# Performance work log

Hardware: AMD Instinct MI355X
Metric: run time of the kernel (lower is better)

Reference implementation:

```python
import jax, jax.numpy as jnp
import numpy as np

B, C_IN, FH, TW = 64, 8, 128, 128
FBINS, A, M_ARR, M_SRC = 257, 360, 4, 2
EPS = 1e-6


def _conv2d(x, w):
    return jax.lax.conv_general_dilated(x, w, (1, 1), 'SAME', dimension_numbers=('NCHW', 'OIHW', 'NCHW'))


def _bn(x, g, b, m, v):
    sh = (1, -1, 1, 1)
    return (x - m.reshape(sh)) * jax.lax.rsqrt(v.reshape(sh) + 1e-5) * g.reshape(sh) + b.reshape(sh)


def _pool2(x):
    b_, c, h, w = x.shape
    return x.reshape(b_, c, h // 2, 2, w // 2, 2).max(axis=(3, 5))


def _block(x, w, g, b, m, v):
    return _pool2(jax.nn.relu(_bn(_conv2d(x, w), g, b, m, v)))


def _conv1d(x, w, b):
    return jax.lax.conv_general_dilated(x, w, (1,), 'SAME', dimension_numbers=('NCH', 'OIH', 'NCH')) + b[None, :, None]


def setup_inputs() -> dict:
    ks = jax.random.split(jax.random.key(0), 16)
    r = lambda i, shp, s=1.0: jax.random.normal(ks[i], shp, dtype=jnp.float32) * s
    d = {
        'X': r(0, (B, C_IN, FH, TW)),
        'sv_real': r(1, (B, FBINS, A, M_ARR)),
        'sv_imag': r(2, (B, FBINS, A, M_ARR)),
        'correlation': jnp.zeros((1,), jnp.float32),
        'conv1_w': r(3, (64, C_IN, 3, 3), 0.1),
        'conv2_w': r(4, (64, 64, 3, 3), 0.04),
        'conv3_w': r(5, (64, 64, 3, 3), 0.04),
        'conv4_w': r(6, (FBINS, 64, 3, 3), 0.04),
        'fc_w': r(7, (32, 64), 0.1),
        'fc_b': jnp.zeros((32,), jnp.float32),
        'convs2_w': r(8, (FBINS, FBINS, 3), 0.02),
        'convs2_b': jnp.zeros((FBINS,), jnp.float32),
        'convs1_w': r(9, (1, FBINS, 3), 0.03),
        'convs1_b': jnp.zeros((1,), jnp.float32),
        'ca_w1': r(10, (16, FBINS), 0.06),
        'ca_w2': r(11, (FBINS, 16), 0.2),
    }
    for i, c in [(1, 64), (2, 64), (3, 64), (4, FBINS)]:
        d[f'bn{i}_g'] = jnp.ones((c,), jnp.float32)
        d[f'bn{i}_b'] = jnp.zeros((c,), jnp.float32)
        d[f'bn{i}_m'] = jnp.zeros((c,), jnp.float32)
        d[f'bn{i}_v'] = jnp.ones((c,), jnp.float32)
    return d


def reference(X, sv_real, sv_imag, correlation,
              conv1_w, bn1_g, bn1_b, bn1_m, bn1_v,
              conv2_w, bn2_g, bn2_b, bn2_m, bn2_v,
              conv3_w, bn3_g, bn3_b, bn3_m, bn3_v,
              conv4_w, bn4_g, bn4_b, bn4_m, bn4_v,
              fc_w, fc_b, convs2_w, convs2_b, convs1_w, convs1_b,
              ca_w1, ca_w2):
    b_ = X.shape[0]
    # CNN encoder: (B,8,128,128) -> (B,257,8,8)
    z = _block(X, conv1_w, bn1_g, bn1_b, bn1_m, bn1_v)
    z = _block(z, conv2_w, bn2_g, bn2_b, bn2_m, bn2_v)
    z = _block(z, conv3_w, bn3_g, bn3_b, bn3_m, bn3_v)
    z = _block(z, conv4_w, bn4_g, bn4_b, bn4_m, bn4_v)
    z = z.reshape(b_, FBINS, -1) @ fc_w.T + fc_b            # (B,257,32)
    z = z.reshape(b_, FBINS, C_IN // 2, C_IN)               # (B,257,4,8)
    Rz = jax.lax.complex(z[..., :M_ARR], z[..., M_ARR:])    # (B,257,4,4)
    # hermitianize + diagonal loading
    Rz = 0.5 * (Rz + jnp.conj(jnp.swapaxes(Rz, -1, -2)))
    Rz = Rz + 1e-5 * jnp.eye(M_ARR, dtype=Rz.dtype)
    _, evecs = jnp.linalg.eigh(Rz)                          # ascending eigenvalues
    Un = evecs[..., ::-1][..., M_SRC:]                      # noise subspace (B,F,4,2)
    UnUnH = Un @ jnp.conj(jnp.swapaxes(Un, -1, -2))         # (B,F,4,4)
    svc = jnp.conj(jax.lax.complex(sv_real, sv_imag))       # (B,F,A,4)
    # faithful to torch code: denom[a] = sum_{m,n} conj(sv[a,m]) UnUnH[m,n] conj(sv[a,n])
    denom = jnp.real(jnp.einsum('bfam,bfmn,bfan->bfa', svc, UnUnH, svc))
    spectrum = 1.0 / jnp.maximum(denom, EPS)                # (B,257,360)
    spectrum = jax.nn.leaky_relu(_conv1d(spectrum, convs2_w, convs2_b), 0.1)
    # channel attention over the 257 freq channels
    y = spectrum.mean(-1)                                   # (B,257)
    att = jax.nn.sigmoid(jax.nn.relu(y @ ca_w1.T) @ ca_w2.T)
    spectrum = spectrum * att[:, :, None]
    spectrum = jax.nn.sigmoid(_conv1d(spectrum, convs1_w, convs1_b))[:, 0, :]  # (B,360)
    # soft-argmax over top-5 peaks
    angles = jnp.linspace(0.0, 360.0, A + 1)[:-1]
    vals, idx = jax.lax.top_k(spectrum, 5)
    wts = jax.nn.softmax(20.0 * vals, axis=-1)
    doa = (wts * angles[idx]).sum(-1)[:, None]              # (B,1)
    return doa, spectrum
```

## Files before the change

### kernel.cpp

```cpp
#include <hip/hip_runtime.h>

typedef unsigned short u16;
typedef unsigned int u32;
typedef short short8 __attribute__((ext_vector_type(8)));
typedef float f32x4 __attribute__((ext_vector_type(4)));

#define NB 64
#define NFB 257
#define NANG 360

__device__ __forceinline__ u16 f2bf(float x) {
    u32 u = __float_as_uint(x);
    u = (u + 0x7fffu + ((u >> 16) & 1u)) >> 16;
    return (u16)u;
}
__device__ __forceinline__ float bf2f(u16 h) { return __uint_as_float(((u32)h) << 16); }

__global__ __launch_bounds__(256) void bnprep(
    const float* g1, const float* b1, const float* m1, const float* v1,
    const float* g2, const float* b2, const float* m2, const float* v2,
    const float* g3, const float* b3, const float* m3, const float* v3,
    const float* g4, const float* b4, const float* m4, const float* v4,
    float* out)
{
    int L = blockIdx.x;
    const float* gs[4] = {g1, g2, g3, g4};
    const float* bs[4] = {b1, b2, b3, b4};
    const float* ms[4] = {m1, m2, m3, m4};
    const float* vs[4] = {v1, v2, v3, v4};
    int n = (L == 3) ? 257 : 64;
    float* sc = out + L * 1024;
    float* bi = sc + 512;
    for (int i = threadIdx.x; i < n; i += 256) {
        float s = gs[L][i] * rsqrtf(vs[L][i] + 1e-5f);
        sc[i] = s;
        bi[i] = bs[L][i] - ms[L][i] * s;
    }
}

__global__ __launch_bounds__(256) void bpack(
    const float* __restrict__ w, u16* __restrict__ Bp,
    int CREAL, int OCREAL, int NT, int KCC, int NFTOT)
{
    int i = blockIdx.x * 256 + threadIdx.x;
    int total = NT * KCC * 2 * NFTOT * 64;
    if (i >= total) return;
    int lane = i & 63;
    int t = i >> 6;
    int nf = t % NFTOT;
    int th = t / NFTOT;
    int h = th & 1;
    int chunk = th >> 1;
    int s = chunk / KCC, kc = chunk % KCC;
    int n = nf * 16 + (lane & 15);
    int k0 = kc * 32 + (lane >> 4) * 8;
    u16 o8[8];
    #pragma unroll
    for (int e = 0; e < 8; ++e) {
        int k = k0 + e;
        float v = 0.f;
        if (k < CREAL && n < OCREAL) v = w[((size_t)n * CREAL + k) * NT + s];
        u16 hh = f2bf(v);
        o8[e] = (h == 0) ? hh : f2bf(v - bf2f(hh));
    }
    u16* d = Bp + (size_t)i * 8;
    #pragma unroll
    for (int e = 0; e < 8; ++e) d[e] = o8[e];
}

__global__ __launch_bounds__(256) void bpack1(const float* __restrict__ w, u16* __restrict__ Bp)
{
    int i = blockIdx.x * 256 + threadIdx.x;
    if (i >= 3 * 2 * 4 * 64) return;
    int lane = i & 63;
    int t = i >> 6;
    int nf = t % 4;
    int th = t / 4;
    int h = th & 1;
    int ky = th >> 1;
    int n = nf * 16 + (lane & 15);
    int q = lane >> 4;
    u16 o8[8];
    #pragma unroll
    for (int e = 0; e < 8; ++e) {
        float v = (q < 3) ? w[((size_t)(n * 8 + e) * 3 + ky) * 3 + q] : 0.f;
        u16 hh = f2bf(v);
        o8[e] = (h == 0) ? hh : f2bf(v - bf2f(hh));
    }
    u16* d = Bp + (size_t)i * 8;
    #pragma unroll
    for (int e = 0; e < 8; ++e) d[e] = o8[e];
}

__global__ __launch_bounds__(256) void xpack_kernel(
    const float* __restrict__ X, u16* __restrict__ hi, u16* __restrict__ lo)
{
    __shared__ float Xs[8][132];
    int bid = blockIdx.x;
    int prow = bid % 130;
    int b = bid / 130;
    bool inr = (prow >= 1 && prow <= 128);
    for (int i = threadIdx.x; i < 8 * 130; i += 256) {
        int c = i / 130, pcol = i % 130;
        float v = 0.f;
        if (inr && pcol >= 1 && pcol <= 128)
            v = X[(((size_t)b * 8 + c) * 128 + (prow - 1)) * 128 + (pcol - 1)];
        Xs[c][pcol] = v;
    }
    __syncthreads();
    for (int p = threadIdx.x; p < 130; p += 256) {
        short8 h8, l8;
        #pragma unroll
        for (int c = 0; c < 8; ++c) {
            float f = Xs[c][p];
            u16 hh = f2bf(f);
            h8[c] = (short)hh;
            l8[c] = (short)f2bf(f - bf2f(hh));
        }
        size_t o = (((size_t)b * 130 + prow) * 130 + p) * 8;
        *(short8*)(hi + o) = h8;
        *(short8*)(lo + o) = l8;
    }
}

__global__ __launch_bounds__(256) void zpad(
    u16* hi, u16* lo, int Bn, int Hp, int Wp, int Cb, int doCols)
{
    int perB = 2 * Wp + (doCols ? 2 * (Hp - 2) : 0);
    long total = (long)Bn * perB * Cb;
    for (long idx = blockIdx.x * 256L + threadIdx.x; idx < total; idx += (long)gridDim.x * 256) {
        int c = (int)(idx % Cb);
        long t = idx / Cb;
        int p = (int)(t % perB);
        int b = (int)(t / perB);
        int row, col;
        if (p < Wp) { row = 0; col = p; }
        else if (p < 2 * Wp) { row = Hp - 1; col = p - Wp; }
        else { int pp = p - 2 * Wp; row = 1 + (pp >> 1); col = (pp & 1) ? (Wp - 1) : 0; }
        size_t o = (((size_t)b * Hp + row) * Wp + col) * Cb + c;
        hi[o] = 0;
        lo[o] = 0;
    }
}

__global__ __launch_bounds__(256) void conv_c1(
    const u16* __restrict__ Ahi, const u16* __restrict__ Alo,
    const u16* __restrict__ Bp,
    const float* __restrict__ esc, const float* __restrict__ ebi,
    u16* __restrict__ Ohi, u16* __restrict__ Olo)
{
    constexpr int Wst = 130, Hp = 130;
    constexpr int SROWS = 5;
    constexpr int SPIX = SROWS * Wst;
    constexpr int PSTR = 48;
    constexpr int STAGEB = SPIX * PSTR;
    constexpr int POOLB = 2 * 128 * 64 * 4;
    __shared__ __align__(16) char sm[POOLB + 64];

    int bid = blockIdx.x;
    int ytile = bid % 64;
    int b = bid / 64;
    int y0 = ytile * 2;
    int tid = threadIdx.x;
    int wv = tid >> 6;
    int l = tid & 63;
    int r = l & 15, q = l >> 4;

    for (int pix = tid; pix < SPIX; pix += 256) {
        int prow = y0 + pix / Wst, pcol = pix % Wst;
        uint4 vh = {0, 0, 0, 0}, vl = {0, 0, 0, 0};
        if (prow < Hp) {
            size_t g = (((size_t)b * Hp + prow) * Wst + pcol) * 16;
            vh = *(const uint4*)((const char*)Ahi + g);
            vl = *(const uint4*)((const char*)Alo + g);
        }
        *(uint4*)(sm + pix * PSTR) = vh;
        *(uint4*)(sm + STAGEB + pix * PSTR) = vl;
    }
    __syncthreads();

    f32x4 acc[4][4];
    #pragma unroll
    for (int mi = 0; mi < 4; ++mi)
        #pragma unroll
        for (int ni = 0; ni < 4; ++ni)
            acc[mi][ni] = (f32x4){0.f, 0.f, 0.f, 0.f};

    #pragma unroll
    for (int ky = 0; ky < 3; ++ky) {
        short8 ah[4], al[4];
        #pragma unroll
        for (int mi = 0; mi < 4; ++mi) {
            int mp0 = (wv * 4 + mi) * 16;
            int mpix = ((mp0 >> 7) + ky) * Wst + (mp0 & 127);
            int off = (mpix + r + q) * PSTR;
            ah[mi] = *(const short8*)(sm + off);
            al[mi] = *(const short8*)(sm + STAGEB + off);
        }
        #pragma unroll
        for (int ni = 0; ni < 4; ++ni) {
            const u16* bt = Bp + ((size_t)(ky * 2) * 4 + ni) * 512 + l * 8;
            short8 bh = *(const short8*)bt;
            short8 bl = *(const short8*)(bt + 4 * 512);
            #pragma unroll
            for (int mi = 0; mi < 4; ++mi) {
                acc[mi][ni] = __builtin_amdgcn_mfma_f32_16x16x32_bf16(ah[mi], bh, acc[mi][ni], 0, 0, 0);
                acc[mi][ni] = __builtin_amdgcn_mfma_f32_16x16x32_bf16(ah[mi], bl, acc[mi][ni], 0, 0, 0);
                acc[mi][ni] = __builtin_amdgcn_mfma_f32_16x16x32_bf16(al[mi], bh, acc[mi][ni], 0, 0, 0);
            }
        }
    }

    __syncthreads();
    float* pt = (float*)sm;
    #pragma unroll
    for (int mi = 0; mi < 4; ++mi)
        #pragma unroll
        for (int ni = 0; ni < 4; ++ni)
            #pragma unroll
            for (int j = 0; j < 4; ++j) {
                int mp = (wv * 4 + mi) * 16 + q * 4 + j;
                pt[mp * 64 + ni * 16 + r] = acc[mi][ni][j];
            }
    __syncthreads();
    for (int i = tid; i < 64 * 64; i += 256) {
        int c = i % 64;
        int x2 = i / 64;
        float sc0 = esc[c], bi0 = ebi[c];
        float m = -3.4e38f;
        #pragma unroll
        for (int dy = 0; dy < 2; ++dy)
            #pragma unroll
            for (int dx = 0; dx < 2; ++dx) {
                float v = fmaf(pt[(dy * 128 + 2 * x2 + dx) * 64 + c], sc0, bi0);
                m = fmaxf(m, v);
            }
        m = fmaxf(m, 0.f);
        size_t o = (((size_t)b * 66 + (y0 / 2 + 1)) * 66 + (x2 + 1)) * 64 + c;
        u16 hh = f2bf(m);
        Ohi[o] = hh;
        Olo[o] = f2bf(m - bf2f(hh));
    }
}

template<int C, int H, int W, int OC, int R, int KH, int KW, int NF, int MFW,
         int PSTR, int OUTMODE, int NFTOT, int CSECT>
__global__ __launch_bounds__(256) void conv_gemm(
    const u16* __restrict__ Ahi, const u16* __restrict__ Alo,
    const u16* __restrict__ Bp,
    const float* __restrict__ esc, const float* __restrict__ ebi,
    u16* __restrict__ Ohi, u16* __restrict__ Olo, float* __restrict__ Of)
{
    constexpr int KCC = (C + 31) / 32;
    constexpr int KCS = KCC / CSECT;
    constexpr int SECB = (C / CSECT) * 2;
    constexpr int CB16 = SECB / 16;
    constexpr int Wst = W + KW - 1;
    constexpr int Hp = H + KH - 1;
    constexpr int SROWS = R + KH - 1;
    constexpr int SPIX = SROWS * Wst;
    constexpr int OCB = NF * 16;
    constexpr int HT = (H + R - 1) / R;
    constexpr int STAGEB = SPIX * PSTR;
    constexpr int POOLB = (OUTMODE == 2) ? 0 : (R * W * OCB * 4);
    constexpr int SMEMB = (2 * STAGEB > POOLB) ? (2 * STAGEB) : POOLB;
    __shared__ __align__(16) char sm[SMEMB + 64];

    int bid = blockIdx.x;
    int ytile = bid % HT;
    int b = bid / HT;
    int tid = threadIdx.x;
    int wv = tid >> 6;
    int l = tid & 63;
    int r = l & 15, q = l >> 4;
    int y0 = ytile * R;

    f32x4 acc[MFW][NF];
    #pragma unroll
    for (int mi = 0; mi < MFW; ++mi)
        #pragma unroll
        for (int ni = 0; ni < NF; ++ni)
            acc[mi][ni] = (f32x4){0.f, 0.f, 0.f, 0.f};

    for (int cs = 0; cs < CSECT; ++cs) {
        __syncthreads();
        for (int i = tid; i < SPIX * CB16; i += 256) {
            int pix = i / CB16, sub = i - pix * CB16;
            int prow = y0 + pix / Wst, pcol = pix % Wst;
            uint4 vh = {0, 0, 0, 0}, vl = {0, 0, 0, 0};
            if (prow < Hp) {
                size_t g = (((size_t)b * Hp + prow) * Wst + pcol) * (size_t)(C * 2)
                         + (size_t)cs * SECB + (size_t)sub * 16;
                vh = *(const uint4*)((const char*)Ahi + g);
                vl = *(const uint4*)((const char*)Alo + g);
            }
            *(uint4*)(sm + pix * PSTR + sub * 16) = vh;
            *(uint4*)(sm + STAGEB + pix * PSTR + sub * 16) = vl;
        }
        __syncthreads();

        for (int s = 0; s < KH * KW; ++s) {
            int ky = s / KW, kx = s % KW;
            #pragma unroll
            for (int kc = 0; kc < KCS; ++kc) {
                int chunk = s * KCC + cs * KCS + kc;
                short8 ah[MFW], al[MFW];
                #pragma unroll
                for (int mi = 0; mi < MFW; ++mi) {
                    int mp0 = (wv * MFW + mi) * 16;
                    int mpix = ((mp0 / W) + ky) * Wst + (mp0 % W) + kx;
                    int off = (mpix + r) * PSTR + q * 16 + kc * 64;
                    ah[mi] = *(const short8*)(sm + off);
                    al[mi] = *(const short8*)(sm + STAGEB + off);
                }
                #pragma unroll
                for (int ni = 0; ni < NF; ++ni) {
                    int nfg = blockIdx.y * NF + ni;
                    const u16* bt = Bp + ((size_t)(chunk * 2) * NFTOT + nfg) * 512 + l * 8;
                    short8 bh = *(const short8*)bt;
                    short8 bl = *(const short8*)(bt + (size_t)NFTOT * 512);
                    #pragma unroll
                    for (int mi = 0; mi < MFW; ++mi) {
                        acc[mi][ni] = __builtin_amdgcn_mfma_f32_16x16x32_bf16(ah[mi], bh, acc[mi][ni], 0, 0, 0);
                        acc[mi][ni] = __builtin_amdgcn_mfma_f32_16x16x32_bf16(ah[mi], bl, acc[mi][ni], 0, 0, 0);
                        acc[mi][ni] = __builtin_amdgcn_mfma_f32_16x16x32_bf16(al[mi], bh, acc[mi][ni], 0, 0, 0);
                    }
                }
            }
        }
    }

    if (OUTMODE == 2) {
        #pragma unroll
        for (int ni = 0; ni < NF; ++ni) {
            int nn = (blockIdx.y * NF + ni) * 16 + r;
            float bi0 = (nn < OC) ? ebi[nn] : 0.f;
            #pragma unroll
            for (int mi = 0; mi < MFW; ++mi) {
                #pragma unroll
                for (int j = 0; j < 4; ++j) {
                    int t = y0 + (wv * MFW + mi) * 16 + q * 4 + j;
                    if (t < H && nn < OC) {
                        float v = acc[mi][ni][j] + bi0;
                        Of[((size_t)b * H + t) * (size_t)OC + nn] = (v >= 0.f) ? v : 0.1f * v;
                    }
                }
            }
        }
    } else {
        __syncthreads();
        float* pt = (float*)sm;
        #pragma unroll
        for (int mi = 0; mi < MFW; ++mi)
            #pragma unroll
            for (int ni = 0; ni < NF; ++ni)
                #pragma unroll
                for (int j = 0; j < 4; ++j) {
                    int mp = (wv * MFW + mi) * 16 + q * 4 + j;
                    pt[mp * OCB + ni * 16 + r] = acc[mi][ni][j];
                }
        __syncthreads();
        constexpr int HO = H / 2, WO = W / 2;
        for (int i = tid; i < (R / 2) * WO * OCB; i += 256) {
            int c = i % OCB;
            int rem = i / OCB;
            int x2 = rem % WO;
            int y2 = rem / WO;
            int oc = blockIdx.y * OCB + c;
            float sc0 = 0.f, bi0 = 0.f;
            if (oc < OC) { sc0 = esc[oc]; bi0 = ebi[oc]; }
            float m = -3.4e38f;
            #pragma unroll
            for (int dy = 0; dy < 2; ++dy)
                #pragma unroll
                for (int dx = 0; dx < 2; ++dx) {
                    float v = fmaf(pt[((2 * y2 + dy) * W + 2 * x2 + dx) * OCB + c], sc0, bi0);
                    m = fmaxf(m, v);
                }
            m = fmaxf(m, 0.f);
            if (OUTMODE == 0) {
                size_t o = (((size_t)b * (HO + 2) + (y0 / 2 + y2 + 1)) * (WO + 2) + (x2 + 1)) * (size_t)OC + oc;
                u16 hh = f2bf(m);
                Ohi[o] = hh;
                Olo[o] = f2bf(m - bf2f(hh));
            } else {
                if (oc < OC)
                    Of[(((size_t)b * HO + (y0 / 2 + y2)) * WO + x2) * (size_t)OC + oc] = m;
            }
        }
    }
}

__global__ __launch_bounds__(512) void convs2_gemm(
    const u16* __restrict__ Ahi, const u16* __restrict__ Alo,
    const u16* __restrict__ Bp, const float* __restrict__ bia,
    float* __restrict__ sp2)
{
    constexpr int SPIX = 386;
    constexpr int PSTR = 80;
    constexpr int STAGEB = SPIX * PSTR;
    __shared__ __align__(16) char sm[2 * STAGEB];

    int b = blockIdx.x;
    int nt = blockIdx.y;
    int tid = threadIdx.x;
    int wv = tid >> 6;
    int l = tid & 63;
    int r = l & 15, q = l >> 4;

    f32x4 acc[3][3];
    #pragma unroll
    for (int mi = 0; mi < 3; ++mi)
        #pragma unroll
        for (int ni = 0; ni < 3; ++ni)
            acc[mi][ni] = (f32x4){0.f, 0.f, 0.f, 0.f};

    for (int cs = 0; cs < 9; ++cs) {
        __syncthreads();
        for (int i = tid; i < SPIX * 4; i += 512) {
            int pix = i >> 2, sub = i & 3;
            uint4 vh = {0, 0, 0, 0}, vl = {0, 0, 0, 0};
            if (pix < 362) {
                size_t g = ((size_t)b * 362 + pix) * 576 + (size_t)cs * 64 + (size_t)sub * 16;
                vh = *(const uint4*)((const char*)Ahi + g);
                vl = *(const uint4*)((const char*)Alo + g);
            }
            *(uint4*)(sm + pix * PSTR + sub * 16) = vh;
            *(uint4*)(sm + STAGEB + pix * PSTR + sub * 16) = vl;
        }
        __syncthreads();

        #pragma unroll
        for (int ky = 0; ky < 3; ++ky) {
            int chunk = ky * 9 + cs;
            short8 bh[3], bl[3];
            #pragma unroll
            for (int ni = 0; ni < 3; ++ni) {
                const u16* bt = Bp + ((size_t)(chunk * 2) * 18 + nt * 3 + ni) * 512 + l * 8;
                bh[ni] = *(const short8*)bt;
                bl[ni] = *(const short8*)(bt + 18 * 512);
            }
            #pragma unroll
            for (int mi = 0; mi < 3; ++mi) {
                int off = ((wv * 3 + mi) * 16 + r + ky) * PSTR + q * 16;
                short8 ah = *(const short8*)(sm + off);
                short8 al = *(const short8*)(sm + STAGEB + off);
                #pragma unroll
                for (int ni = 0; ni < 3; ++ni) {
                    acc[mi][ni] = __builtin_amdgcn_mfma_f32_16x16x32_bf16(ah, bh[ni], acc[mi][ni], 0, 0, 0);
                    acc[mi][ni] = __builtin_amdgcn_mfma_f32_16x16x32_bf16(ah, bl[ni], acc[mi][ni], 0, 0, 0);
                    acc[mi][ni] = __builtin_amdgcn_mfma_f32_16x16x32_bf16(al, bh[ni], acc[mi][ni], 0, 0, 0);
                }
            }
        }
    }

    #pragma unroll
    for (int ni = 0; ni < 3; ++ni) {
        int n = (nt * 3 + ni) * 16 + r;
        if (n >= NFB) continue;
        float bi0 = bia[n];
        #pragma unroll
        for (int mi = 0; mi < 3; ++mi) {
            int t0 = (wv * 3 + mi) * 16 + q * 4;
            #pragma unroll
            for (int j = 0; j < 4; ++j) {
                int t = t0 + j;
                if (t < NANG) {
                    float v = acc[mi][ni][j] + bi0;
                    sp2[((size_t)b * NANG + t) * NFB + n] = (v >= 0.f) ? v : 0.1f * v;
                }
            }
        }
    }
}

__global__ __launch_bounds__(256) void fc_kernel(
    const float* __restrict__ z, const float* __restrict__ fw,
    const float* __restrict__ fb, float* __restrict__ zfc)
{
    int bid = blockIdx.x;
    int ftile = bid % 33;
    int b = bid / 33;
    int j = threadIdx.x & 31;
    int f = ftile * 8 + (threadIdx.x >> 5);
    if (f >= 257) return;
    const float* zb = z + (size_t)b * 16448;
    float a = fb[j];
    #pragma unroll 8
    for (int s = 0; s < 64; ++s) a = fmaf(zb[s * 257 + f], fw[j * 64 + s], a);
    zfc[((size_t)b * 257 + f) * 32 + j] = a;
}

__global__ __launch_bounds__(64) void eigh_kernel(const float* __restrict__ z, double* __restrict__ rp)
{
    int idx = blockIdx.x * 64 + threadIdx.x;
    if (idx >= NB * NFB) return;
    const float* zr = z + (size_t)idx * 32;
    double Ar[4][4], Ai[4][4], Vr[4][4], Vi[4][4];
    #pragma unroll
    for (int m = 0; m < 4; ++m)
        #pragma unroll
        for (int n = 0; n < 4; ++n) {
            Ar[m][n] = 0.5 * ((double)zr[m * 8 + n] + (double)zr[n * 8 + m]);
            Ai[m][n] = 0.5 * ((double)zr[m * 8 + n + 4] - (double)zr[n * 8 + m + 4]);
            Vr[m][n] = (m == n) ? 1.0 : 0.0;
            Vi[m][n] = 0.0;
        }
    #pragma unroll
    for (int m = 0; m < 4; ++m) Ar[m][m] += 1e-5;

    for (int sweep = 0; sweep < 8; ++sweep) {
        #pragma unroll
        for (int p = 0; p < 3; ++p)
            #pragma unroll
            for (int qq = p + 1; qq < 4; ++qq) {
                double apr = Ar[p][qq], api = Ai[p][qq];
                double rmod = sqrt(apr * apr + api * api);
                if (rmod < 1e-300) continue;
                double cph = apr / rmod, sph = api / rmod;
                double tau = (Ar[qq][qq] - Ar[p][p]) / (2.0 * rmod);
                double t = (tau >= 0.0) ? (-1.0 / (tau + sqrt(1.0 + tau * tau)))
                                        : (1.0 / (-tau + sqrt(1.0 + tau * tau)));
                double c = 1.0 / sqrt(1.0 + t * t);
                double s = t * c;
                double wr = s * cph, wi = s * sph;
                #pragma unroll
                for (int i = 0; i < 4; ++i) {
                    double xr = Ar[i][p], xi = Ai[i][p];
                    double yr = Ar[i][qq], yi = Ai[i][qq];
                    Ar[i][p] = c * xr + (wr * yr + wi * yi);
                    Ai[i][p] = c * xi + (wr * yi - wi * yr);
                    Ar[i][qq] = c * yr - (wr * xr - wi * xi);
                    Ai[i][qq] = c * yi - (wr * xi + wi * xr);
                }
                #pragma unroll
                for (int i = 0; i < 4; ++i) {
                    double xr = Ar[p][i], xi = Ai[p][i];
                    double yr = Ar[qq][i], yi = Ai[qq][i];
                    Ar[p][i] = c * xr + (wr * yr - wi * yi);
                    Ai[p][i] = c * xi + (wr * yi + wi * yr);
                    Ar[qq][i] = c * yr - (wr * xr + wi * xi);
                    Ai[qq][i] = c * yi - (wr * xi - wi * xr);
                }
                #pragma unroll
                for (int i = 0; i < 4; ++i) {
                    double xr = Vr[i][p], xi = Vi[i][p];
                    double yr = Vr[i][qq], yi = Vi[i][qq];
                    Vr[i][p] = c * xr + (wr * yr + wi * yi);
                    Vi[i][p] = c * xi + (wr * yi - wi * yr);
                    Vr[i][qq] = c * yr - (wr * xr - wi * xi);
                    Vi[i][qq] = c * yi - (wr * xi + wi * xr);
                }
            }
    }
    double ev[4] = {Ar[0][0], Ar[1][1], Ar[2][2], Ar[3][3]};
    int i0 = 0;
    #pragma unroll
    for (int k = 1; k < 4; ++k) if (ev[k] < ev[i0]) i0 = k;
    int i1 = (i0 == 0) ? 1 : 0;
    #pragma unroll
    for (int k = 0; k < 4; ++k) if (k != i0 && ev[k] < ev[i1]) i1 = k;
    double* o = rp + (size_t)idx * 16;
    #pragma unroll
    for (int m = 0; m < 4; ++m)
        #pragma unroll
        for (int n = 0; n < 4; ++n)
            o[m * 4 + n] = Vr[m][i0] * Vr[n][i0] + Vi[m][i0] * Vi[n][i0]
                         + Vr[m][i1] * Vr[n][i1] + Vi[m][i1] * Vi[n][i1];
}

__global__ __launch_bounds__(256) void music_kernel(
    const float4* __restrict__ svr, const float4* __restrict__ svi,
    const double* __restrict__ rp, u16* __restrict__ muhi, u16* __restrict__ mulo)
{
    __shared__ double P[32][16];
    __shared__ float T[32][33];
    int bid = blockIdx.x;
    int at = bid % 12; bid /= 12;
    int ft = bid % 9;
    int b = bid / 9;
    int f0 = ft * 32, a0 = at * 32;
    int tid = threadIdx.x;
    for (int i = tid; i < 32 * 16; i += 256) {
        int fi = i >> 4, j = i & 15;
        int f = f0 + fi;
        P[fi][j] = (f < 257) ? rp[((size_t)b * 257 + f) * 16 + j] : 0.0;
    }
    __syncthreads();
    int asub = tid & 31, fsub = tid >> 5;
    int a = a0 + asub;
    #pragma unroll
    for (int k2 = 0; k2 < 4; ++k2) {
        int fl = fsub + 8 * k2;
        int f = f0 + fl;
        float val = 0.f;
        if (a < 360 && f < 257) {
            float4 u = svr[((size_t)b * 257 + f) * 360 + a];
            float4 w = svi[((size_t)b * 257 + f) * 360 + a];
            const double* Pf = P[fl];
            double ua[4] = {u.x, u.y, u.z, u.w};
            double wa[4] = {w.x, w.y, w.z, w.w};
            double qa = 0.0, qb = 0.0;
            #pragma unroll
            for (int m = 0; m < 4; ++m)
                #pragma unroll
                for (int n = 0; n < 4; ++n) {
                    double pmn = Pf[m * 4 + n];
                    qa += pmn * ua[m] * ua[n];
                    qb += pmn * wa[m] * wa[n];
                }
            double den = qa - qb;
            val = (float)(1.0 / fmax(den, 1e-6));
        }
        T[asub][fl] = val;
    }
    __syncthreads();
    #pragma unroll
    for (int p = 0; p < 4; ++p) {
        int row = p * 8 + (tid >> 5);
        int fc = tid & 31;
        int a2 = a0 + row;
        if (a2 < 360) {
            float v = T[row][fc];
            size_t o = (((size_t)b * 362) + a2 + 1) * 288 + f0 + fc;
            u16 hh = f2bf(v);
            muhi[o] = hh;
            mulo[o] = f2bf(v - bf2f(hh));
        }
    }
}

__global__ __launch_bounds__(256) void attn_partial(const float* __restrict__ sp2, float* __restrict__ part)
{
    int bid = blockIdx.x;
    int ch = bid % 6;
    int b = bid / 6;
    int t0 = ch * 60;
    for (int f = threadIdx.x; f < 257; f += 256) {
        float s = 0.f;
        for (int t = 0; t < 60; ++t) s += sp2[((size_t)b * 360 + t0 + t) * 257 + f];
        part[((size_t)b * 6 + ch) * 257 + f] = s;
    }
}

__global__ __launch_bounds__(256) void attn_finish(
    const float* __restrict__ part, const float* __restrict__ w1,
    const float* __restrict__ w2, float* __restrict__ att)
{
    __shared__ float ys[257];
    __shared__ float hs[16];
    int b = blockIdx.x;
    int tid = threadIdx.x;
    for (int f = tid; f < 257; f += 256) {
        float s = 0.f;
        #pragma unroll
        for (int c = 0; c < 6; ++c) s += part[((size_t)b * 6 + c) * 257 + f];
        ys[f] = s * (1.0f / 360.0f);
    }
    __syncthreads();
    if (tid < 16) {
        float h = 0.f;
        for (int c = 0; c < 257; ++c) h = fmaf(ys[c], w1[(size_t)tid * 257 + c], h);
        hs[tid] = fmaxf(h, 0.f);
    }
    __syncthreads();
    for (int o = tid; o < 257; o += 256) {
        float a = 0.f;
        #pragma unroll
        for (int j = 0; j < 16; ++j) a = fmaf(hs[j], w2[(size_t)o * 16 + j], a);
        att[(size_t)b * 257 + o] = 1.0f / (1.0f + expf(-a));
    }
}

__global__ __launch_bounds__(256) void convs1_kernel(
    const float* __restrict__ sp2, const float* __restrict__ att,
    const float* __restrict__ w, const float* __restrict__ bb,
    float* __restrict__ outS)
{
    int bid = blockIdx.x;
    int tt = bid % 90;
    int b = bid / 90;
    int wv = threadIdx.x >> 6, l = threadIdx.x & 63;
    int t = tt * 4 + wv;
    float s = 0.f;
    for (int f = l; f < 257; f += 64) {
        float av = att[(size_t)b * 257 + f];
        float w0 = w[f * 3] * av, w1 = w[f * 3 + 1] * av, w2 = w[f * 3 + 2] * av;
        const float* col = sp2 + (size_t)b * 360 * 257 + f;
        if (t > 0)   s = fmaf(w0, col[(size_t)(t - 1) * 257], s);
        s = fmaf(w1, col[(size_t)t * 257], s);
        if (t < 359) s = fmaf(w2, col[(size_t)(t + 1) * 257], s);
    }
    #pragma unroll
    for (int off = 32; off > 0; off >>= 1) s += __shfl_down(s, off, 64);
    if (l == 0) outS[(size_t)b * 360 + t] = 1.0f / (1.0f + expf(-(s + bb[0])));
}

__global__ __launch_bounds__(64) void doa_kernel(const float* __restrict__ spec, float* __restrict__ doa)
{
    int b = blockIdx.x;
    int l = threadIdx.x;
    const float* s = spec + (size_t)b * NANG;
    float v[6];
    #pragma unroll
    for (int j = 0; j < 6; ++j) {
        int idx = l + 64 * j;
        v[j] = (idx < NANG) ? s[idx] : -3.4e38f;
    }
    float wvv[5]; int wii[5];
    #pragma unroll
    for (int k = 0; k < 5; ++k) {
        float bv = v[0]; int bj = 0;
        #pragma unroll
        for (int j = 1; j < 6; ++j)
            if (v[j] > bv) { bv = v[j]; bj = j; }
        int bi = l + 64 * bj;
        #pragma unroll
        for (int off = 1; off < 64; off <<= 1) {
            float ov = __shfl_xor(bv, off, 64);
            int oi = __shfl_xor(bi, off, 64);
            if (ov > bv || (ov == bv && oi < bi)) { bv = ov; bi = oi; }
        }
        wvv[k] = bv; wii[k] = bi;
        if ((bi & 63) == l) {
            int j = bi >> 6;
            #pragma unroll
            for (int jj = 0; jj < 6; ++jj)
                if (jj == j) v[jj] = -3.4e38f;
        }
    }
    if (l == 0) {
        float m = wvv[0];
        float wsum = 0.f, asum = 0.f;
        #pragma unroll
        for (int k = 0; k < 5; ++k) {
            float e = expf(20.0f * (wvv[k] - m));
            wsum += e;
            asum += e * (float)wii[k];
        }
        doa[b] = asum / wsum;
    }
}

extern "C" void kernel_launch(void* const* d_in, const int* in_sizes, int n_in,
                              void* d_out, int out_size, void* d_ws, size_t ws_size,
                              hipStream_t stream)
{
    const float* X    = (const float*)d_in[0];
    const float* svr  = (const float*)d_in[1];
    const float* svi  = (const float*)d_in[2];
    const float* c1w  = (const float*)d_in[4];
    const float* c2w  = (const float*)d_in[5];
    const float* c3w  = (const float*)d_in[6];
    const float* c4w  = (const float*)d_in[7];
    const float* fcw  = (const float*)d_in[8];
    const float* fcb  = (const float*)d_in[9];
    const float* s2w  = (const float*)d_in[10];
    const float* s2b  = (const float*)d_in[11];
    const float* s1w  = (const float*)d_in[12];
    const float* s1b  = (const float*)d_in[13];
    const float* caw1 = (const float*)d_in[14];
    const float* caw2 = (const float*)d_in[15];
    const float* bn1g = (const float*)d_in[16]; const float* bn1b = (const float*)d_in[17];
    const float* bn1m = (const float*)d_in[18]; const float* bn1v = (const float*)d_in[19];
    const float* bn2g = (const float*)d_in[20]; const float* bn2b = (const float*)d_in[21];
    const float* bn2m = (const float*)d_in[22]; const float* bn2v = (const float*)d_in[23];
    const float* bn3g = (const float*)d_in[24]; const float* bn3b = (const float*)d_in[25];
    const float* bn3m = (const float*)d_in[26]; const float* bn3v = (const float*)d_in[27];
    const float* bn4g = (const float*)d_in[28]; const float* bn4b = (const float*)d_in[29];
    const float* bn4m = (const float*)d_in[30]; const float* bn4v = (const float*)d_in[31];

    char* wsb = (char*)d_ws;
    u16* xp_hi = (u16*)(wsb + 0);
    u16* xp_lo = (u16*)(wsb + 17305600);
    u16* c3_hi = (u16*)(wsb + 0);
    u16* c3_lo = (u16*)(wsb + 9469952);
    u16* mu_hi = (u16*)(wsb + 0);
    u16* mu_lo = (u16*)(wsb + 13344768);
    const size_t Bb = 34611200;
    u16*   c2_hi = (u16*)(wsb + Bb);
    u16*   c2_lo = (u16*)(wsb + Bb + 35684352);
    float*  zbuf = (float*)(wsb + Bb);
    float*  zfc  = (float*)(wsb + Bb + 4210688);
    double* rp   = (double*)(wsb + Bb + 6316032);
    float*  sp2  = (float*)(wsb + Bb + 8421376);
    float*  part = (float*)(wsb + Bb + 32106496);
    float*  att  = (float*)(wsb + Bb + 32501248);
    const size_t Cb = Bb + 71368704;
    u16* c4_hi = (u16*)(wsb + Cb);
    u16* c4_lo = (u16*)(wsb + Cb + 2654208);
    u16* bp1 = (u16*)(wsb + Cb + 5308416);
    u16* bp2 = (u16*)(wsb + Cb + 5382144);
    u16* bp3 = (u16*)(wsb + Cb + 5529600);
    u16* bp4 = (u16*)(wsb + Cb + 5677056);
    u16* bp5 = (u16*)(wsb + Cb + 6414336);
    float* bns = (float*)(wsb + Cb + 7409664);

    float* outD = (float*)d_out;
    float* outS = (float*)d_out + 64;

    bnprep<<<4, 256, 0, stream>>>(bn1g, bn1b, bn1m, bn1v, bn2g, bn2b, bn2m, bn2v,
                                  bn3g, bn3b, bn3m, bn3v, bn4g, bn4b, bn4m, bn4v, bns);
    bpack1<<<6, 256, 0, stream>>>(c1w, bp1);
    bpack<<<36, 256, 0, stream>>>(c2w, bp2, 64, 64, 9, 2, 4);
    bpack<<<36, 256, 0, stream>>>(c3w, bp3, 64, 64, 9, 2, 4);
    bpack<<<180, 256, 0, stream>>>(c4w, bp4, 64, 257, 9, 2, 20);
    bpack<<<243, 256, 0, stream>>>(s2w, bp5, 257, 257, 3, 9, 18);
    xpack_kernel<<<64 * 130, 256, 0, stream>>>(X, xp_hi, xp_lo);
    zpad<<<4161, 256, 0, stream>>>(c2_hi, c2_lo, 64, 66, 66, 64, 1);
    zpad<<<1088, 256, 0, stream>>>(c4_hi, c4_lo, 64, 18, 18, 64, 1);

    conv_c1<<<64 * 64, 256, 0, stream>>>(xp_hi, xp_lo, bp1, bns, bns + 512, c2_hi, c2_lo);
    zpad<<<2112, 256, 0, stream>>>(c3_hi, c3_lo, 64, 34, 34, 64, 1);
    conv_gemm<64, 64, 64, 64, 2, 3, 3, 4, 2, 144, 0, 4, 1>
        <<<dim3(64 * 32, 1), 256, 0, stream>>>(c2_hi, c2_lo, bp2, bns + 1024, bns + 1536, c3_hi, c3_lo, nullptr);
    conv_gemm<64, 32, 32, 64, 4, 3, 3, 4, 2, 144, 0, 4, 1>
        <<<dim3(64 * 8, 1), 256, 0, stream>>>(c3_hi, c3_lo, bp3, bns + 2048, bns + 2560, c4_hi, c4_lo, nullptr);
    zpad<<<144, 256, 0, stream>>>(mu_hi, mu_lo, 64, 362, 1, 288, 0);
    conv_gemm<64, 16, 16, 257, 8, 3, 3, 4, 2, 144, 1, 20, 1>
        <<<dim3(64 * 2, 5), 256, 0, stream>>>(c4_hi, c4_lo, bp4, bns + 3072, bns + 3584, nullptr, nullptr, zbuf);

    fc_kernel<<<64 * 33, 256, 0, stream>>>(zbuf, fcw, fcb, zfc);
    eigh_kernel<<<NFB, 64, 0, stream>>>(zfc, rp);
    music_kernel<<<64 * 108, 256, 0, stream>>>((const float4*)svr, (const float4*)svi, rp, mu_hi, mu_lo);
    convs2_gemm<<<dim3(64, 6), 512, 0, stream>>>(mu_hi, mu_lo, bp5, s2b, sp2);

    attn_partial<<<64 * 6, 256, 0, stream>>>(sp2, part);
    attn_finish<<<64, 256, 0, stream>>>(part, caw1, caw2, att);
    convs1_kernel<<<64 * 90, 256, 0, stream>>>(sp2, att, s1w, s1b, outS);
    doa_kernel<<<64, 64, 0, stream>>>(outS, outD);
}
```

Before: 457.0 us.

## Remap conv MFMA tiles for in-register pooling, swizzle LDS, double-buffer B fragments

The conv kernels now assign each wave's M-fragments to matching 2x2 pooling windows, so BN+ReLU+maxpool is done directly from accumulators. This removes the shared-memory staging round trip and its extra barriers. LDS staging uses a dense 64-byte pixel stride with an XOR swizzle instead of padded strides, shrinking shared memory and avoiding bank conflicts. Weight fragments are double-buffered in registers, so the next chunk's global loads overlap the current MFMAs, at the cost of higher register pressure. The generic conv template is specialized to 3x3 with C=64.

```diff
diff --git a/kernel.cpp b/kernel.cpp
--- a/kernel.cpp
+++ b/kernel.cpp
@@ -152,10 +152,8 @@
     constexpr int Wst = 130, Hp = 130;
     constexpr int SROWS = 5;
     constexpr int SPIX = SROWS * Wst;
-    constexpr int PSTR = 48;
-    constexpr int STAGEB = SPIX * PSTR;
-    constexpr int POOLB = 2 * 128 * 64 * 4;
-    __shared__ __align__(16) char sm[POOLB + 64];
+    constexpr int STAGEB = SPIX * 16;
+    __shared__ __align__(16) char sm[2 * STAGEB];
 
     int bid = blockIdx.x;
     int ytile = bid % 64;
@@ -174,97 +172,81 @@
             vh = *(const uint4*)((const char*)Ahi + g);
             vl = *(const uint4*)((const char*)Alo + g);
         }
-        *(uint4*)(sm + pix * PSTR) = vh;
-        *(uint4*)(sm + STAGEB + pix * PSTR) = vl;
+        *(uint4*)(sm + pix * 16) = vh;
+        *(uint4*)(sm + STAGEB + pix * 16) = vl;
     }
     __syncthreads();
 
-    f32x4 acc[4][4];
-    #pragma unroll
-    for (int mi = 0; mi < 4; ++mi)
-        #pragma unroll
-        for (int ni = 0; ni < 4; ++ni)
-            acc[mi][ni] = (f32x4){0.f, 0.f, 0.f, 0.f};
+    f32x4 acc[4][4] = {};
 
     #pragma unroll
     for (int ky = 0; ky < 3; ++ky) {
-        short8 ah[4], al[4];
-        #pragma unroll
-        for (int mi = 0; mi < 4; ++mi) {
-            int mp0 = (wv * 4 + mi) * 16;
-            int mpix = ((mp0 >> 7) + ky) * Wst + (mp0 & 127);
-            int off = (mpix + r + q) * PSTR;
-            ah[mi] = *(const short8*)(sm + off);
-            al[mi] = *(const short8*)(sm + STAGEB + off);
-        }
+        short8 bh[4], bl[4];
         #pragma unroll
         for (int ni = 0; ni < 4; ++ni) {
             const u16* bt = Bp + ((size_t)(ky * 2) * 4 + ni) * 512 + l * 8;
-            short8 bh = *(const short8*)bt;
-            short8 bl = *(const short8*)(bt + 4 * 512);
+            bh[ni] = *(const short8*)bt;
+            bl[ni] = *(const short8*)(bt + 4 * 512);
+        }
+        short8 ah[4], al[4];
+        #pragma unroll
+        for (int mi = 0; mi < 4; ++mi) {
+            int pf = wv * 2 + (mi >> 1);
+            int y = mi & 1;
+            int p = (y + ky) * Wst + pf * 16 + r + q;
+            ah[mi] = *(const short8*)(sm + p * 16);
+            al[mi] = *(const short8*)(sm + STAGEB + p * 16);
+        }
+        #pragma unroll
+        for (int ni = 0; ni < 4; ++ni)
             #pragma unroll
             for (int mi = 0; mi < 4; ++mi) {
-                acc[mi][ni] = __builtin_amdgcn_mfma_f32_16x16x32_bf16(ah[mi], bh, acc[mi][ni], 0, 0, 0);
-                acc[mi][ni] = __builtin_amdgcn_mfma_f32_16x16x32_bf16(ah[mi], bl, acc[mi][ni], 0, 0, 0);
-                acc[mi][ni] = __builtin_amdgcn_mfma_f32_16x16x32_bf16(al[mi], bh, acc[mi][ni], 0, 0, 0);
-            }
-        }
-    }
-
-    __syncthreads();
-    float* pt = (float*)sm;
-    #pragma unroll
-    for (int mi = 0; mi < 4; ++mi)
-        #pragma unroll
-        for (int ni = 0; ni < 4; ++ni)
-            #pragma unroll
-            for (int j = 0; j < 4; ++j) {
-                int mp = (wv * 4 + mi) * 16 + q * 4 + j;
-                pt[mp * 64 + ni * 16 + r] = acc[mi][ni][j];
-            }
-    __syncthreads();
-    for (int i = tid; i < 64 * 64; i += 256) {
-        int c = i % 64;
-        int x2 = i / 64;
-        float sc0 = esc[c], bi0 = ebi[c];
-        float m = -3.4e38f;
-        #pragma unroll
-        for (int dy = 0; dy < 2; ++dy)
-            #pragma unroll
-            for (int dx = 0; dx < 2; ++dx) {
-                float v = fmaf(pt[(dy * 128 + 2 * x2 + dx) * 64 + c], sc0, bi0);
-                m = fmaxf(m, v);
-            }
-        m = fmaxf(m, 0.f);
-        size_t o = (((size_t)b * 66 + (y0 / 2 + 1)) * 66 + (x2 + 1)) * 64 + c;
-        u16 hh = f2bf(m);
-        Ohi[o] = hh;
-        Olo[o] = f2bf(m - bf2f(hh));
-    }
-}
-
-template<int C, int H, int W, int OC, int R, int KH, int KW, int NF, int MFW,
-         int PSTR, int OUTMODE, int NFTOT, int CSECT>
+                acc[mi][ni] = __builtin_amdgcn_mfma_f32_16x16x32_bf16(ah[mi], bh[ni], acc[mi][ni], 0, 0, 0);
+                acc[mi][ni] = __builtin_amdgcn_mfma_f32_16x16x32_bf16(ah[mi], bl[ni], acc[mi][ni], 0, 0, 0);
+                acc[mi][ni] = __builtin_amdgcn_mfma_f32_16x16x32_bf16(al[mi], bh[ni], acc[mi][ni], 0, 0, 0);
+            }
+    }
+
+    #pragma unroll
+    for (int ni = 0; ni < 4; ++ni) {
+        int oc = ni * 16 + r;
+        float sc0 = esc[oc], bi0 = ebi[oc];
+        #pragma unroll
+        for (int pi = 0; pi < 2; ++pi) {
+            int pf = wv * 2 + pi;
+            #pragma unroll
+            for (int k = 0; k < 2; ++k) {
+                float m = -3.4e38f;
+                #pragma unroll
+                for (int dmi = 0; dmi < 2; ++dmi)
+                    #pragma unroll
+                    for (int dj = 0; dj < 2; ++dj)
+                        m = fmaxf(m, fmaf(acc[2 * pi + dmi][ni][2 * k + dj], sc0, bi0));
+                m = fmaxf(m, 0.f);
+                int x2 = pf * 8 + q * 2 + k;
+                size_t o = (((size_t)b * 66 + (y0 / 2 + 1)) * 66 + (x2 + 1)) * 64 + oc;
+                u16 hh = f2bf(m);
+                Ohi[o] = hh;
+                Olo[o] = f2bf(m - bf2f(hh));
+            }
+        }
+    }
+}
+
+template<int H, int W, int OC, int R, int NF, int MFW, int OUTMODE, int NFTOT>
 __global__ __launch_bounds__(256) void conv_gemm(
     const u16* __restrict__ Ahi, const u16* __restrict__ Alo,
     const u16* __restrict__ Bp,
     const float* __restrict__ esc, const float* __restrict__ ebi,
     u16* __restrict__ Ohi, u16* __restrict__ Olo, float* __restrict__ Of)
 {
-    constexpr int KCC = (C + 31) / 32;
-    constexpr int KCS = KCC / CSECT;
-    constexpr int SECB = (C / CSECT) * 2;
-    constexpr int CB16 = SECB / 16;
-    constexpr int Wst = W + KW - 1;
-    constexpr int Hp = H + KH - 1;
-    constexpr int SROWS = R + KH - 1;
+    constexpr int Wst = W + 2, Hp = H + 2;
+    constexpr int SROWS = R + 2;
     constexpr int SPIX = SROWS * Wst;
-    constexpr int OCB = NF * 16;
-    constexpr int HT = (H + R - 1) / R;
-    constexpr int STAGEB = SPIX * PSTR;
-    constexpr int POOLB = (OUTMODE == 2) ? 0 : (R * W * OCB * 4);
-    constexpr int SMEMB = (2 * STAGEB > POOLB) ? (2 * STAGEB) : POOLB;
-    __shared__ __align__(16) char sm[SMEMB + 64];
+    constexpr int XF = W / 16;
+    constexpr int STAGEB = SPIX * 64;
+    constexpr int HT = H / R;
+    __shared__ __align__(16) char sm[2 * STAGEB];
 
     int bid = blockIdx.x;
     int ytile = bid % HT;
@@ -274,118 +256,95 @@
     int l = tid & 63;
     int r = l & 15, q = l >> 4;
     int y0 = ytile * R;
-
-    f32x4 acc[MFW][NF];
-    #pragma unroll
-    for (int mi = 0; mi < MFW; ++mi)
-        #pragma unroll
-        for (int ni = 0; ni < NF; ++ni)
-            acc[mi][ni] = (f32x4){0.f, 0.f, 0.f, 0.f};
-
-    for (int cs = 0; cs < CSECT; ++cs) {
+    int nfg0 = blockIdx.y * NF;
+
+    f32x4 acc[MFW][NF] = {};
+    short8 Bh[2][NF], Bl[2][NF];
+
+    auto loadB = [&](int buf, int chunk) {
+        #pragma unroll
+        for (int ni = 0; ni < NF; ++ni) {
+            const u16* bt = Bp + ((size_t)(chunk * 2) * NFTOT + nfg0 + ni) * 512 + l * 8;
+            Bh[buf][ni] = *(const short8*)bt;
+            Bl[buf][ni] = *(const short8*)(bt + (size_t)NFTOT * 512);
+        }
+    };
+    loadB(0, 0);
+
+    #pragma unroll
+    for (int cs = 0; cs < 2; ++cs) {
         __syncthreads();
-        for (int i = tid; i < SPIX * CB16; i += 256) {
-            int pix = i / CB16, sub = i - pix * CB16;
+        for (int i = tid; i < SPIX * 4; i += 256) {
+            int pix = i >> 2, sub = i & 3;
             int prow = y0 + pix / Wst, pcol = pix % Wst;
             uint4 vh = {0, 0, 0, 0}, vl = {0, 0, 0, 0};
             if (prow < Hp) {
-                size_t g = (((size_t)b * Hp + prow) * Wst + pcol) * (size_t)(C * 2)
-                         + (size_t)cs * SECB + (size_t)sub * 16;
+                size_t g = (((size_t)b * Hp + prow) * Wst + pcol) * 128 + cs * 64 + sub * 16;
                 vh = *(const uint4*)((const char*)Ahi + g);
                 vl = *(const uint4*)((const char*)Alo + g);
             }
-            *(uint4*)(sm + pix * PSTR + sub * 16) = vh;
-            *(uint4*)(sm + STAGEB + pix * PSTR + sub * 16) = vl;
+            int dst = (pix << 6) + ((sub ^ ((pix >> 1) & 3)) << 4);
+            *(uint4*)(sm + dst) = vh;
+            *(uint4*)(sm + STAGEB + dst) = vl;
         }
         __syncthreads();
 
-        for (int s = 0; s < KH * KW; ++s) {
-            int ky = s / KW, kx = s % KW;
-            #pragma unroll
-            for (int kc = 0; kc < KCS; ++kc) {
-                int chunk = s * KCC + cs * KCS + kc;
-                short8 ah[MFW], al[MFW];
+        #pragma unroll
+        for (int s = 0; s < 9; ++s) {
+            int cur = (cs * 9 + s) & 1;
+            if (s < 8) loadB(cur ^ 1, (s + 1) * 2 + cs);
+            else if (cs == 0) loadB(cur ^ 1, 1);
+            int ky = s / 3, kx = s % 3;
+            short8 ah[MFW], al[MFW];
+            #pragma unroll
+            for (int mi = 0; mi < MFW; ++mi) {
+                int pf = wv * (MFW / 2) + (mi >> 1);
+                int y = (pf / XF) * 2 + (mi & 1);
+                int xf = pf % XF;
+                int p = (y + ky) * Wst + xf * 16 + kx + r;
+                int off = (p << 6) + ((q ^ ((p >> 1) & 3)) << 4);
+                ah[mi] = *(const short8*)(sm + off);
+                al[mi] = *(const short8*)(sm + STAGEB + off);
+            }
+            #pragma unroll
+            for (int ni = 0; ni < NF; ++ni)
                 #pragma unroll
                 for (int mi = 0; mi < MFW; ++mi) {
-                    int mp0 = (wv * MFW + mi) * 16;
-                    int mpix = ((mp0 / W) + ky) * Wst + (mp0 % W) + kx;
-                    int off = (mpix + r) * PSTR + q * 16 + kc * 64;
-                    ah[mi] = *(const short8*)(sm + off);
-                    al[mi] = *(const short8*)(sm + STAGEB + off);
+                    acc[mi][ni] = __builtin_amdgcn_mfma_f32_16x16x32_bf16(ah[mi], Bh[cur][ni], acc[mi][ni], 0, 0, 0);
+                    acc[mi][ni] = __builtin_amdgcn_mfma_f32_16x16x32_bf16(ah[mi], Bl[cur][ni], acc[mi][ni], 0, 0, 0);
+                    acc[mi][ni] = __builtin_amdgcn_mfma_f32_16x16x32_bf16(al[mi], Bh[cur][ni], acc[mi][ni], 0, 0, 0);
                 }
+        }
+    }
+
+    #pragma unroll
+    for (int ni = 0; ni < NF; ++ni) {
+        int oc = (nfg0 + ni) * 16 + r;
+        float sc0 = esc[oc], bi0 = ebi[oc];
+        #pragma unroll
+        for (int pi = 0; pi < MFW / 2; ++pi) {
+            int pf = wv * (MFW / 2) + pi;
+            int y2 = y0 / 2 + pf / XF;
+            int xb = (pf % XF) * 8 + q * 2;
+            #pragma unroll
+            for (int k = 0; k < 2; ++k) {
+                float m = -3.4e38f;
                 #pragma unroll
-                for (int ni = 0; ni < NF; ++ni) {
-                    int nfg = blockIdx.y * NF + ni;
-                    const u16* bt = Bp + ((size_t)(chunk * 2) * NFTOT + nfg) * 512 + l * 8;
-                    short8 bh = *(const short8*)bt;
-                    short8 bl = *(const short8*)(bt + (size_t)NFTOT * 512);
+                for (int dmi = 0; dmi < 2; ++dmi)
                     #pragma unroll
-                    for (int mi = 0; mi < MFW; ++mi) {
-                        acc[mi][ni] = __builtin_amdgcn_mfma_f32_16x16x32_bf16(ah[mi], bh, acc[mi][ni], 0, 0, 0);
-                        acc[mi][ni] = __builtin_amdgcn_mfma_f32_16x16x32_bf16(ah[mi], bl, acc[mi][ni], 0, 0, 0);
-                        acc[mi][ni] = __builtin_amdgcn_mfma_f32_16x16x32_bf16(al[mi], bh, acc[mi][ni], 0, 0, 0);
-                    }
+                    for (int dj = 0; dj < 2; ++dj)
+                        m = fmaxf(m, fmaf(acc[2 * pi + dmi][ni][2 * k + dj], sc0, bi0));
+                m = fmaxf(m, 0.f);
+                int x2 = xb + k;
+                if (OUTMODE == 0) {
+                    size_t o = (((size_t)b * (H / 2 + 2) + y2 + 1) * (W / 2 + 2) + (x2 + 1)) * 64 + oc;
+                    u16 hh = f2bf(m);
+                    Ohi[o] = hh;
+                    Olo[o] = f2bf(m - bf2f(hh));
+                } else {
+                    if (oc < OC)
+                        Of[(((size_t)b * (H / 2) + y2) * (W / 2) + x2) * (size_t)OC + oc] = m;
                 }
-            }
-        }
-    }
-
-    if (OUTMODE == 2) {
-        #pragma unroll
-        for (int ni = 0; ni < NF; ++ni) {
-            int nn = (blockIdx.y * NF + ni) * 16 + r;
-            float bi0 = (nn < OC) ? ebi[nn] : 0.f;
-            #pragma unroll
-            for (int mi = 0; mi < MFW; ++mi) {
-                #pragma unroll
-                for (int j = 0; j < 4; ++j) {
-                    int t = y0 + (wv * MFW + mi) * 16 + q * 4 + j;
-                    if (t < H && nn < OC) {
-                        float v = acc[mi][ni][j] + bi0;
-                        Of[((size_t)b * H + t) * (size_t)OC + nn] = (v >= 0.f) ? v : 0.1f * v;
-                    }
-                }
-            }
-        }
-    } else {
-        __syncthreads();
-        float* pt = (float*)sm;
-        #pragma unroll
-        for (int mi = 0; mi < MFW; ++mi)
-            #pragma unroll
-            for (int ni = 0; ni < NF; ++ni)
-                #pragma unroll
-                for (int j = 0; j < 4; ++j) {
-                    int mp = (wv * MFW + mi) * 16 + q * 4 + j;
-                    pt[mp * OCB + ni * 16 + r] = acc[mi][ni][j];
-                }
-        __syncthreads();
-        constexpr int HO = H / 2, WO = W / 2;
-        for (int i = tid; i < (R / 2) * WO * OCB; i += 256) {
-            int c = i % OCB;
-            int rem = i / OCB;
-            int x2 = rem % WO;
-            int y2 = rem / WO;
-            int oc = blockIdx.y * OCB + c;
-            float sc0 = 0.f, bi0 = 0.f;
-            if (oc < OC) { sc0 = esc[oc]; bi0 = ebi[oc]; }
-            float m = -3.4e38f;
-            #pragma unroll
-            for (int dy = 0; dy < 2; ++dy)
-                #pragma unroll
-                for (int dx = 0; dx < 2; ++dx) {
-                    float v = fmaf(pt[((2 * y2 + dy) * W + 2 * x2 + dx) * OCB + c], sc0, bi0);
-                    m = fmaxf(m, v);
-                }
-            m = fmaxf(m, 0.f);
-            if (OUTMODE == 0) {
-                size_t o = (((size_t)b * (HO + 2) + (y0 / 2 + y2 + 1)) * (WO + 2) + (x2 + 1)) * (size_t)OC + oc;
-                u16 hh = f2bf(m);
-                Ohi[o] = hh;
-                Olo[o] = f2bf(m - bf2f(hh));
-            } else {
-                if (oc < OC)
-                    Of[(((size_t)b * HO + (y0 / 2 + y2)) * WO + x2) * (size_t)OC + oc] = m;
             }
         }
     }
@@ -397,8 +356,7 @@
     float* __restrict__ sp2)
 {
     constexpr int SPIX = 386;
-    constexpr int PSTR = 80;
-    constexpr int STAGEB = SPIX * PSTR;
+    constexpr int STAGEB = SPIX * 64;
     __shared__ __align__(16) char sm[2 * STAGEB];
 
     int b = blockIdx.x;
@@ -408,13 +366,20 @@
     int l = tid & 63;
     int r = l & 15, q = l >> 4;
 
-    f32x4 acc[3][3];
-    #pragma unroll
-    for (int mi = 0; mi < 3; ++mi)
-        #pragma unroll
-        for (int ni = 0; ni < 3; ++ni)
-            acc[mi][ni] = (f32x4){0.f, 0.f, 0.f, 0.f};
-
+    f32x4 acc[3][3] = {};
+    short8 Bh[2][3], Bl[2][3];
+
+    auto loadB = [&](int buf, int chunk) {
+        #pragma unroll
+        for (int ni = 0; ni < 3; ++ni) {
+            const u16* bt = Bp + ((size_t)(chunk * 2) * 18 + nt * 3 + ni) * 512 + l * 8;
+            Bh[buf][ni] = *(const short8*)bt;
+            Bl[buf][ni] = *(const short8*)(bt + 18 * 512);
+        }
+    };
+    loadB(0, 0);
+
+    #pragma unroll
     for (int cs = 0; cs < 9; ++cs) {
         __syncthreads();
         for (int i = tid; i < SPIX * 4; i += 512) {
@@ -425,31 +390,28 @@
                 vh = *(const uint4*)((const char*)Ahi + g);
                 vl = *(const uint4*)((const char*)Alo + g);
             }
-            *(uint4*)(sm + pix * PSTR + sub * 16) = vh;
-            *(uint4*)(sm + STAGEB + pix * PSTR + sub * 16) = vl;
+            int dst = (pix << 6) + ((sub ^ ((pix >> 1) & 3)) << 4);
+            *(uint4*)(sm + dst) = vh;
+            *(uint4*)(sm + STAGEB + dst) = vl;
         }
         __syncthreads();
 
         #pragma unroll
         for (int ky = 0; ky < 3; ++ky) {
-            int chunk = ky * 9 + cs;
-            short8 bh[3], bl[3];
-            #pragma unroll
-            for (int ni = 0; ni < 3; ++ni) {
-                const u16* bt = Bp + ((size_t)(chunk * 2) * 18 + nt * 3 + ni) * 512 + l * 8;
-                bh[ni] = *(const short8*)bt;
-                bl[ni] = *(const short8*)(bt + 18 * 512);
-            }
+            int cur = (cs * 3 + ky) & 1;
+            if (ky < 2) loadB(cur ^ 1, (ky + 1) * 9 + cs);
+            else if (cs < 8) loadB(cur ^ 1, cs + 1);
             #pragma unroll
             for (int mi = 0; mi < 3; ++mi) {
-                int off = ((wv * 3 + mi) * 16 + r + ky) * PSTR + q * 16;
+                int p = (wv * 3 + mi) * 16 + r + ky;
+                int off = (p << 6) + ((q ^ ((p >> 1) & 3)) << 4);
                 short8 ah = *(const short8*)(sm + off);
                 short8 al = *(const short8*)(sm + STAGEB + off);
                 #pragma unroll
                 for (int ni = 0; ni < 3; ++ni) {
-                    acc[mi][ni] = __builtin_amdgcn_mfma_f32_16x16x32_bf16(ah, bh[ni], acc[mi][ni], 0, 0, 0);
-                    acc[mi][ni] = __builtin_amdgcn_mfma_f32_16x16x32_bf16(ah, bl[ni], acc[mi][ni], 0, 0, 0);
-                    acc[mi][ni] = __builtin_amdgcn_mfma_f32_16x16x32_bf16(al, bh[ni], acc[mi][ni], 0, 0, 0);
+                    acc[mi][ni] = __builtin_amdgcn_mfma_f32_16x16x32_bf16(ah, Bh[cur][ni], acc[mi][ni], 0, 0, 0);
+                    acc[mi][ni] = __builtin_amdgcn_mfma_f32_16x16x32_bf16(ah, Bl[cur][ni], acc[mi][ni], 0, 0, 0);
+                    acc[mi][ni] = __builtin_amdgcn_mfma_f32_16x16x32_bf16(al, Bh[cur][ni], acc[mi][ni], 0, 0, 0);
                 }
             }
         }
@@ -813,12 +775,12 @@
 
     conv_c1<<<64 * 64, 256, 0, stream>>>(xp_hi, xp_lo, bp1, bns, bns + 512, c2_hi, c2_lo);
     zpad<<<2112, 256, 0, stream>>>(c3_hi, c3_lo, 64, 34, 34, 64, 1);
-    conv_gemm<64, 64, 64, 64, 2, 3, 3, 4, 2, 144, 0, 4, 1>
+    conv_gemm<64, 64, 64, 2, 4, 2, 0, 4>
         <<<dim3(64 * 32, 1), 256, 0, stream>>>(c2_hi, c2_lo, bp2, bns + 1024, bns + 1536, c3_hi, c3_lo, nullptr);
-    conv_gemm<64, 32, 32, 64, 4, 3, 3, 4, 2, 144, 0, 4, 1>
+    conv_gemm<32, 32, 64, 4, 4, 2, 0, 4>
         <<<dim3(64 * 8, 1), 256, 0, stream>>>(c3_hi, c3_lo, bp3, bns + 2048, bns + 2560, c4_hi, c4_lo, nullptr);
     zpad<<<144, 256, 0, stream>>>(mu_hi, mu_lo, 64, 362, 1, 288, 0);
-    conv_gemm<64, 16, 16, 257, 8, 3, 3, 4, 2, 144, 1, 20, 1>
+    conv_gemm<16, 16, 257, 8, 4, 2, 1, 20>
         <<<dim3(64 * 2, 5), 256, 0, stream>>>(c4_hi, c4_lo, bp4, bns + 3072, bns + 3584, nullptr, nullptr, zbuf);
 
     fc_kernel<<<64 * 33, 256, 0, stream>>>(zbuf, fcw, fcb, zfc);
```

After: 428.6 us. -6.2%, faster.
